# Performance work log

Hardware: AMD Instinct MI355X
Metric: run time of the kernel (lower is better)

## Reference

```python
import jax, jax.numpy as jnp
import numpy as np
from jax import lax

B, N, M = 4, 8192, 8192  # batch, source points, target points


def setup_inputs() -> dict:
    key = jax.random.key(0)
    k1, k2 = jax.random.split(key)
    source = jax.random.normal(k1, (B, N, 3), dtype=jnp.float32)
    target = jax.random.normal(k2, (B, M, 3), dtype=jnp.float32)
    return {"source_point_cloud": source, "target_point_cloud": target}


def reference(source_point_cloud, target_point_cloud):
    src, tgt = source_point_cloud, target_point_cloud
    # validity masks replace move_zero_point's data-dependent filtering
    valid_s = jnp.any(src != 0.0, axis=-1)  # [B, N]
    valid_t = jnp.any(tgt != 0.0, axis=-1)  # [B, M]

    # nearest neighbor via brute force: argmin_m ||s_n - t_m||^2
    # ||s||^2 is constant per row, so argmin over (||t||^2 - 2 s.t)
    t_sq = jnp.sum(tgt * tgt, axis=-1)                       # [B, M]
    dots = jnp.einsum('bnd,bmd->bnm', src, tgt)              # [B, N, M]
    d = t_sq[:, None, :] - 2.0 * dots                        # [B, N, M]
    d = jnp.where(valid_t[:, None, :], d, jnp.inf)
    idx = jnp.argmin(lax.stop_gradient(d), axis=-1)          # [B, N] int

    nn = jnp.take_along_axis(tgt, idx[..., None], axis=1)    # [B, N, 3]
    sq = jnp.sum((src - nn) ** 2, axis=-1)                   # [B, N]
    w = valid_s.astype(src.dtype)
    cnt = jnp.maximum(jnp.sum(w, axis=-1), 1.0)              # valid points per batch
    per_batch = jnp.sum(sq * w, axis=-1) / (3.0 * cnt)       # MSELoss mean over N*3
    return jnp.mean(per_batch)
```

## Files before the change

### kernel.cpp

```cpp
#include <hip/hip_runtime.h>

#define NBATCH 4
#define NPTS   8192
#define MTGT   8192
#define BN     (NBATCH*NPTS)
#define NCHUNK 8
#define SGRP   32

typedef __attribute__((ext_vector_type(8)))  short bf16x8;
typedef __attribute__((ext_vector_type(16))) float f32x16;

__device__ __forceinline__ unsigned short f2bf(float x) {
    unsigned u = __float_as_uint(x);
    return (unsigned short)((u + 0x7fffu + ((u >> 16) & 1u)) >> 16);
}
__device__ __forceinline__ float bf2f(unsigned short h) {
    return __uint_as_float(((unsigned)h) << 16);
}

__global__ __launch_bounds__(256) void prep_kernel(const float* __restrict__ src,
                                                   const float* __restrict__ tgt,
                                                   unsigned short* __restrict__ Apk,
                                                   unsigned short* __restrict__ Bpk) {
    const int i = blockIdx.x * 256 + threadIdx.x;
    const int T = i >> 5, l = i & 31;
    const unsigned ONE = 0x3F80u;

    float sx = src[3*(size_t)i], sy = src[3*(size_t)i+1], sz = src[3*(size_t)i+2];
    float axf = -2.f*sx, ayf = -2.f*sy, azf = -2.f*sz;
    unsigned axh = f2bf(axf), ayh = f2bf(ayf), azh = f2bf(azf);
    unsigned axl = f2bf(axf - bf2f(axh));
    unsigned ayl = f2bf(ayf - bf2f(ayh));
    unsigned azl = f2bf(azf - bf2f(azh));
    uint4* a0 = (uint4*)(Apk + ((size_t)T*64 +      l) * 8);
    uint4* a1 = (uint4*)(Apk + ((size_t)T*64 + 32 + l) * 8);
    *a0 = make_uint4(axh | (ayh<<16), azh | (axl<<16), ayl | (azl<<16), axh | (ayh<<16));
    *a1 = make_uint4(azh | (ONE<<16), ONE | (ONE<<16), 0u, 0u);

    float tx = tgt[3*(size_t)i], ty = tgt[3*(size_t)i+1], tz = tgt[3*(size_t)i+2];
    unsigned txh = f2bf(tx), tyh = f2bf(ty), tzh = f2bf(tz);
    unsigned txl = f2bf(tx - bf2f(txh));
    unsigned tyl = f2bf(ty - bf2f(tyh));
    unsigned tzl = f2bf(tz - bf2f(tzh));
    float tsq = fmaf(tx, tx, fmaf(ty, ty, tz * tz));
    bool valid = (tx != 0.f) || (ty != 0.f) || (tz != 0.f);
    unsigned qh, qm, ql;
    if (valid) {
        qh = f2bf(tsq);
        float r1 = tsq - bf2f(qh); qm = f2bf(r1);
        float r2 = r1 - bf2f(qm);  ql = f2bf(r2);
    } else { qh = f2bf(1e30f); qm = 0u; ql = 0u; }
    uint4* b0 = (uint4*)(Bpk + ((size_t)T*64 +      l) * 8);
    uint4* b1 = (uint4*)(Bpk + ((size_t)T*64 + 32 + l) * 8);
    *b0 = make_uint4(txh | (tyh<<16), tzh | (txh<<16), tyh | (tzh<<16), txl | (tyl<<16));
    *b1 = make_uint4(tzl | (qh<<16), qm | (ql<<16), 0u, 0u);
}

__device__ __forceinline__ float min16(const f32x16& d, float acc) {
    float r0 = fminf(fminf(d[0],  d[1]),  d[2]);
    float r1 = fminf(fminf(d[3],  d[4]),  d[5]);
    float r2 = fminf(fminf(d[6],  d[7]),  d[8]);
    float r3 = fminf(fminf(d[9],  d[10]), d[11]);
    float r4 = fminf(fminf(d[12], d[13]), d[14]);
    float s0 = fminf(fminf(r0, r1), r2);
    float s1 = fminf(fminf(r3, r4), d[15]);
    return fminf(fminf(s0, s1), acc);
}

__global__ __launch_bounds__(256, 4) void nn_mfma_kernel(const unsigned short* __restrict__ Apk,
                                                         const unsigned short* __restrict__ Bpk,
                                                         float* __restrict__ wspart) {
    __shared__ uint4 ldsB[2048];

    const int tid  = threadIdx.x;
    const int lane = tid & 63, wid = tid >> 6;
    const int sg = blockIdx.x, cy = blockIdx.y, bz = blockIdx.z;

    const bf16x8* Ap = (const bf16x8*)Apk;

    const int Tb0 = bz * 256 + cy * 32;
    const uint4* gB = (const uint4*)(Bpk + (size_t)Tb0 * 512);
#pragma unroll
    for (int j = 0; j < 8; ++j)
        ldsB[j * 256 + tid] = gB[j * 256 + tid];

    const int Ts0 = bz * 256 + sg * 8 + wid * 2;
    bf16x8 s0 = Ap[(size_t)Ts0 * 64 + lane];
    bf16x8 s1 = Ap[(size_t)(Ts0 + 1) * 64 + lane];

    f32x16 z;
#pragma unroll
    for (int e = 0; e < 16; ++e) z[e] = 0.f;
    float acc0 = 3e38f, acc1 = 3e38f;

    __syncthreads();
    const bf16x8* bp = (const bf16x8*)ldsB;

#pragma unroll 2
    for (int m = 0; m < 32; m += 2) {
        bf16x8 tfA = bp[m * 64 + lane];
        bf16x8 tfB = bp[(m + 1) * 64 + lane];
        f32x16 d0 = __builtin_amdgcn_mfma_f32_32x32x16_bf16(tfA, s0, z, 0, 0, 0);
        f32x16 d1 = __builtin_amdgcn_mfma_f32_32x32x16_bf16(tfA, s1, z, 0, 0, 0);
        f32x16 d2 = __builtin_amdgcn_mfma_f32_32x32x16_bf16(tfB, s0, z, 0, 0, 0);
        f32x16 d3 = __builtin_amdgcn_mfma_f32_32x32x16_bf16(tfB, s1, z, 0, 0, 0);
        acc0 = min16(d0, acc0);
        acc1 = min16(d1, acc1);
        acc0 = min16(d2, acc0);
        acc1 = min16(d3, acc1);
    }

    float f0 = fminf(acc0, __shfl_xor(acc0, 32));
    float f1 = fminf(acc1, __shfl_xor(acc1, 32));

    if (lane < 32) {
        float* wb = wspart + (size_t)cy * BN + (size_t)bz * NPTS + sg * 256 + wid * 64;
        wb[lane]      = f0;
        wb[32 + lane] = f1;
    }
}

__global__ __launch_bounds__(256) void reduce_kernel(const float* __restrict__ src,
                                                     const float* __restrict__ wspart,
                                                     double* __restrict__ partials) {
    const int blk = blockIdx.x, tid = threadIdx.x;
    const int gid = blk * 256 + tid;

    float m = 3e38f;
#pragma unroll
    for (int c = 0; c < NCHUNK; ++c) m = fminf(m, wspart[(size_t)c * BN + gid]);

    float sx = src[3*(size_t)gid], sy = src[3*(size_t)gid+1], sz = src[3*(size_t)gid+2];
    bool valid = (sx != 0.f) || (sy != 0.f) || (sz != 0.f);
    float ssq = fmaf(sx, sx, fmaf(sy, sy, sz * sz));
    float sq = fmaxf(0.f, ssq + m);

    __shared__ double sh[512];
    sh[tid] = valid ? (double)sq : 0.0;
    sh[256 + tid] = valid ? 1.0 : 0.0;
    __syncthreads();
    for (int s = 128; s > 0; s >>= 1) {
        if (tid < s) { sh[tid] += sh[tid + s]; sh[256 + tid] += sh[256 + tid + s]; }
        __syncthreads();
    }
    if (tid == 0) { partials[2 * blk] = sh[0]; partials[2 * blk + 1] = sh[256]; }
}

__global__ void final_kernel(const double* __restrict__ partials, float* __restrict__ out) {
    __shared__ double bmv[4];
    int t = threadIdx.x;
    if (t < 4) {
        double s = 0.0, c = 0.0;
        for (int i = 0; i < 32; ++i) {
            s += partials[2 * (t * 32 + i)];
            c += partials[2 * (t * 32 + i) + 1];
        }
        if (c < 1.0) c = 1.0;
        bmv[t] = s / (3.0 * c);
    }
    __syncthreads();
    if (t == 0) out[0] = (float)((bmv[0] + bmv[1] + bmv[2] + bmv[3]) * 0.25);
}

extern "C" void kernel_launch(void* const* d_in, const int* in_sizes, int n_in,
                              void* d_out, int out_size, void* d_ws, size_t ws_size,
                              hipStream_t stream) {
    const float* src = (const float*)d_in[0];
    const float* tgt = (const float*)d_in[1];
    float* out = (float*)d_out;

    unsigned short* Apk = (unsigned short*)d_ws;
    unsigned short* Bpk = (unsigned short*)((char*)d_ws + (1u << 20));
    float* wspart       = (float*)((char*)d_ws + (2u << 20));
    double* partials    = (double*)((char*)d_ws + (3u << 20));

    prep_kernel<<<dim3(BN / 256), dim3(256), 0, stream>>>(src, tgt, Apk, Bpk);
    nn_mfma_kernel<<<dim3(SGRP, NCHUNK, NBATCH), dim3(256), 0, stream>>>(Apk, Bpk, wspart);
    reduce_kernel<<<dim3(BN / 256), dim3(256), 0, stream>>>(src, wspart, partials);
    final_kernel<<<dim3(1), dim3(64), 0, stream>>>(partials, out);
}
```

Before: 22.37 us.

## Fuse bf16 packing of source and target into the MFMA nearest-neighbor kernel

Removes the separate prep kernel and its global workspace round trip. Each block now reads raw float target points with vectorized loads, splits them into bf16 hi/lo fragments and writes them straight into LDS. Each wave builds its source MFMA fragments in registers. This saves one launch and the packed-buffer traffic, at the cost of recomputing the packing redundantly across blocks (each target chunk is packed by 32 blocks and each source tile by 8).

```diff
diff --git a/kernel.cpp b/kernel.cpp
--- a/kernel.cpp
+++ b/kernel.cpp
@@ -18,26 +18,19 @@
     return __uint_as_float(((unsigned)h) << 16);
 }
 
-__global__ __launch_bounds__(256) void prep_kernel(const float* __restrict__ src,
-                                                   const float* __restrict__ tgt,
-                                                   unsigned short* __restrict__ Apk,
-                                                   unsigned short* __restrict__ Bpk) {
-    const int i = blockIdx.x * 256 + threadIdx.x;
-    const int T = i >> 5, l = i & 31;
-    const unsigned ONE = 0x3F80u;
+__device__ __forceinline__ float min16(const f32x16& d, float acc) {
+    float r0 = fminf(fminf(d[0],  d[1]),  d[2]);
+    float r1 = fminf(fminf(d[3],  d[4]),  d[5]);
+    float r2 = fminf(fminf(d[6],  d[7]),  d[8]);
+    float r3 = fminf(fminf(d[9],  d[10]), d[11]);
+    float r4 = fminf(fminf(d[12], d[13]), d[14]);
+    float s0 = fminf(fminf(r0, r1), r2);
+    float s1 = fminf(fminf(r3, r4), d[15]);
+    return fminf(fminf(s0, s1), acc);
+}
 
-    float sx = src[3*(size_t)i], sy = src[3*(size_t)i+1], sz = src[3*(size_t)i+2];
-    float axf = -2.f*sx, ayf = -2.f*sy, azf = -2.f*sz;
-    unsigned axh = f2bf(axf), ayh = f2bf(ayf), azh = f2bf(azf);
-    unsigned axl = f2bf(axf - bf2f(axh));
-    unsigned ayl = f2bf(ayf - bf2f(ayh));
-    unsigned azl = f2bf(azf - bf2f(azh));
-    uint4* a0 = (uint4*)(Apk + ((size_t)T*64 +      l) * 8);
-    uint4* a1 = (uint4*)(Apk + ((size_t)T*64 + 32 + l) * 8);
-    *a0 = make_uint4(axh | (ayh<<16), azh | (axl<<16), ayl | (azl<<16), axh | (ayh<<16));
-    *a1 = make_uint4(azh | (ONE<<16), ONE | (ONE<<16), 0u, 0u);
-
-    float tx = tgt[3*(size_t)i], ty = tgt[3*(size_t)i+1], tz = tgt[3*(size_t)i+2];
+__device__ __forceinline__ void packB(float tx, float ty, float tz,
+                                      uint4& b0, uint4& b1) {
     unsigned txh = f2bf(tx), tyh = f2bf(ty), tzh = f2bf(tz);
     unsigned txl = f2bf(tx - bf2f(txh));
     unsigned tyl = f2bf(ty - bf2f(tyh));
@@ -50,43 +43,57 @@
         float r1 = tsq - bf2f(qh); qm = f2bf(r1);
         float r2 = r1 - bf2f(qm);  ql = f2bf(r2);
     } else { qh = f2bf(1e30f); qm = 0u; ql = 0u; }
-    uint4* b0 = (uint4*)(Bpk + ((size_t)T*64 +      l) * 8);
-    uint4* b1 = (uint4*)(Bpk + ((size_t)T*64 + 32 + l) * 8);
-    *b0 = make_uint4(txh | (tyh<<16), tzh | (txh<<16), tyh | (tzh<<16), txl | (tyl<<16));
-    *b1 = make_uint4(tzl | (qh<<16), qm | (ql<<16), 0u, 0u);
+    b0 = make_uint4(txh | (tyh<<16), tzh | (txh<<16), tyh | (tzh<<16), txl | (tyl<<16));
+    b1 = make_uint4(tzl | (qh<<16), qm | (ql<<16), 0u, 0u);
 }
 
-__device__ __forceinline__ float min16(const f32x16& d, float acc) {
-    float r0 = fminf(fminf(d[0],  d[1]),  d[2]);
-    float r1 = fminf(fminf(d[3],  d[4]),  d[5]);
-    float r2 = fminf(fminf(d[6],  d[7]),  d[8]);
-    float r3 = fminf(fminf(d[9],  d[10]), d[11]);
-    float r4 = fminf(fminf(d[12], d[13]), d[14]);
-    float s0 = fminf(fminf(r0, r1), r2);
-    float s1 = fminf(fminf(r3, r4), d[15]);
-    return fminf(fminf(s0, s1), acc);
-}
-
-__global__ __launch_bounds__(256, 4) void nn_mfma_kernel(const unsigned short* __restrict__ Apk,
-                                                         const unsigned short* __restrict__ Bpk,
+__global__ __launch_bounds__(256, 4) void nn_mfma_kernel(const float* __restrict__ src,
+                                                         const float* __restrict__ tgt,
                                                          float* __restrict__ wspart) {
     __shared__ uint4 ldsB[2048];
 
     const int tid  = threadIdx.x;
     const int lane = tid & 63, wid = tid >> 6;
     const int sg = blockIdx.x, cy = blockIdx.y, bz = blockIdx.z;
+    const unsigned ONE = 0x3F80u;
 
-    const bf16x8* Ap = (const bf16x8*)Apk;
-
-    const int Tb0 = bz * 256 + cy * 32;
-    const uint4* gB = (const uint4*)(Bpk + (size_t)Tb0 * 512);
+    {
+        const float4* tv = reinterpret_cast<const float4*>(
+            tgt + ((size_t)bz * MTGT + (size_t)cy * 1024 + tid * 4) * 3);
+        float4 r0 = tv[0], r1 = tv[1], r2 = tv[2];
+        float px[4] = {r0.x, r0.w, r1.z, r2.y};
+        float py[4] = {r0.y, r1.x, r1.w, r2.z};
+        float pz[4] = {r0.z, r1.y, r2.x, r2.w};
 #pragma unroll
-    for (int j = 0; j < 8; ++j)
-        ldsB[j * 256 + tid] = gB[j * 256 + tid];
+        for (int j = 0; j < 4; ++j) {
+            uint4 b0, b1;
+            packB(px[j], py[j], pz[j], b0, b1);
+            const int q = tid * 4 + j, m = q >> 5, l = q & 31;
+            ldsB[m * 64 + l]      = b0;
+            ldsB[m * 64 + 32 + l] = b1;
+        }
+    }
 
     const int Ts0 = bz * 256 + sg * 8 + wid * 2;
-    bf16x8 s0 = Ap[(size_t)Ts0 * 64 + lane];
-    bf16x8 s1 = Ap[(size_t)(Ts0 + 1) * 64 + lane];
+    bf16x8 s0, s1;
+    {
+        const int half = lane >> 5;
+#pragma unroll
+        for (int t = 0; t < 2; ++t) {
+            const size_t i = (size_t)(Ts0 + t) * 32 + (lane & 31);
+            float sx = src[3*i], sy = src[3*i+1], sz = src[3*i+2];
+            float axf = -2.f*sx, ayf = -2.f*sy, azf = -2.f*sz;
+            unsigned axh = f2bf(axf), ayh = f2bf(ayf), azh = f2bf(azf);
+            unsigned axl = f2bf(axf - bf2f(axh));
+            unsigned ayl = f2bf(ayf - bf2f(ayh));
+            unsigned azl = f2bf(azf - bf2f(azh));
+            uint4 a0 = make_uint4(axh | (ayh<<16), azh | (axl<<16),
+                                  ayl | (azl<<16), axh | (ayh<<16));
+            uint4 a1 = make_uint4(azh | (ONE<<16), ONE | (ONE<<16), 0u, 0u);
+            uint4 frag = half ? a1 : a0;
+            if (t == 0) s0 = *(bf16x8*)&frag; else s1 = *(bf16x8*)&frag;
+        }
+    }
 
     f32x16 z;
 #pragma unroll
@@ -169,13 +176,10 @@
     const float* tgt = (const float*)d_in[1];
     float* out = (float*)d_out;
 
-    unsigned short* Apk = (unsigned short*)d_ws;
-    unsigned short* Bpk = (unsigned short*)((char*)d_ws + (1u << 20));
-    float* wspart       = (float*)((char*)d_ws + (2u << 20));
-    double* partials    = (double*)((char*)d_ws + (3u << 20));
+    float* wspart    = (float*)d_ws;
+    double* partials = (double*)((char*)d_ws + (1u << 20));
 
-    prep_kernel<<<dim3(BN / 256), dim3(256), 0, stream>>>(src, tgt, Apk, Bpk);
-    nn_mfma_kernel<<<dim3(SGRP, NCHUNK, NBATCH), dim3(256), 0, stream>>>(Apk, Bpk, wspart);
+    nn_mfma_kernel<<<dim3(SGRP, NCHUNK, NBATCH), dim3(256), 0, stream>>>(src, tgt, wspart);
     reduce_kernel<<<dim3(BN / 256), dim3(256), 0, stream>>>(src, wspart, partials);
     final_kernel<<<dim3(1), dim3(64), 0, stream>>>(partials, out);
 }
```

New measurement: 17.98 us. 1.24x faster.
